# Kernel optimization log

Hardware: AMD Instinct MI355X
Metric: run time of the kernel (lower is better)

Reference implementation:

```python
import jax, jax.numpy as jnp
import numpy as np

NUM_HEADS = 4

def setup_inputs() -> dict:
    key = jax.random.key(0)
    ks = jax.random.split(key, 5)
    B, H, W, C = 4, 64, 64, 256
    x = jax.random.normal(ks[0], (B, H, W, C), dtype=jnp.float32)
    w_qkv = jax.random.normal(ks[1], (C, 3 * C), dtype=jnp.float32) * (C ** -0.5)
    b_qkv = jax.random.normal(ks[2], (3 * C,), dtype=jnp.float32) * 0.02
    w_out = jax.random.normal(ks[3], (C, C), dtype=jnp.float32) * (C ** -0.5)
    b_out = jax.random.normal(ks[4], (C,), dtype=jnp.float32) * 0.02
    return {"x": x, "w_qkv": w_qkv, "b_qkv": b_qkv, "w_out": w_out, "b_out": b_out}

def reference(x, w_qkv, b_qkv, w_out, b_out):
    B, H, W, C = x.shape
    nh = NUM_HEADS
    hd = C // nh
    scale = hd ** -0.5
    N = H * W
    # qkv projection: [B, N, 3, nh, hd]
    qkv = (x.reshape(B, N, C) @ w_qkv + b_qkv).reshape(B, N, 3, nh, hd)
    q, k, v = jnp.moveaxis(qkv, 2, 0)          # each [B, N, nh, hd]
    q = jnp.swapaxes(q, 1, 2)                  # [B, nh, N, hd]
    k = jnp.swapaxes(k, 1, 2)
    v = jnp.swapaxes(v, 1, 2)
    attn = jax.nn.softmax(jnp.einsum('bhnd,bhmd->bhnm', q * scale, k), axis=-1)
    o = jnp.einsum('bhnm,bhmd->bhnd', attn, v)  # [B, nh, N, hd]
    o = jnp.swapaxes(o, 1, 2).reshape(B, H, W, C)
    return o @ w_out + b_out
```

## Files before the change

### kernel.cpp

```cpp
#include <hip/hip_runtime.h>
#include <stdint.h>

typedef unsigned short u16;
typedef __attribute__((ext_vector_type(8))) short bf16x8;
typedef __attribute__((ext_vector_type(2))) float f32x2;
typedef __attribute__((ext_vector_type(4))) float f32x4;
typedef __attribute__((ext_vector_type(16))) float f32x16;

#define QSCL 0.1803368801111244f

#define GLD_LDS16(g, l) __builtin_amdgcn_global_load_lds( \
    (const __attribute__((address_space(1))) void*)(g),    \
    (__attribute__((address_space(3))) void*)(l), 16, 0, 0)

#if __has_builtin(__builtin_amdgcn_exp2f)
#define EXP2(x) __builtin_amdgcn_exp2f(x)
#else
#define EXP2(x) __builtin_exp2f(x)
#endif

__device__ __forceinline__ u16 f2bf(float f) {
    union { uint32_t i; float f; } v; v.f = f;
    uint32_t i = v.i;
    return (u16)((i + 0x7FFFu + ((i >> 16) & 1u)) >> 16);
}

__device__ __forceinline__ void p32swap(uint32_t& a, uint32_t& b) {
#if __has_builtin(__builtin_amdgcn_permlane32_swap)
    auto r = __builtin_amdgcn_permlane32_swap(a, b, false, false);
    a = (uint32_t)r[0]; b = (uint32_t)r[1];
#else
    const int hh = (int)((threadIdx.x & 63) >> 5);
    uint32_t ta = (uint32_t)__shfl_xor((int)a, 32);
    uint32_t tb = (uint32_t)__shfl_xor((int)b, 32);
    uint32_t na = hh ? tb : a;
    uint32_t nb = hh ? b : ta;
    a = na; b = nb;
#endif
}

__device__ __forceinline__ bf16x8 mk8(uint32_t a, uint32_t b, uint32_t c, uint32_t d) {
    union { uint32_t u[4]; bf16x8 v; } x;
    x.u[0] = a; x.u[1] = b; x.u[2] = c; x.u[3] = d;
    return x.v;
}

__device__ __forceinline__ void transpose_body(const float* __restrict__ src,
                                               u16* __restrict__ dst,
                                               int R, int Ctiles, int bid) {
    __shared__ u16 T[64][68];
    const int t = threadIdx.x;
    const int rt = bid / Ctiles;
    const int ct = bid % Ctiles;
    const int C = Ctiles << 6;

    for (int i = 0; i < 4; i++) {
        int idx = t + 256 * i;
        int row = idx >> 4;
        int col4 = (idx & 15) << 2;
        float4 d = *(const float4*)(src + (size_t)(rt * 64 + row) * C + ct * 64 + col4);
        T[col4 + 0][row] = f2bf(d.x);
        T[col4 + 1][row] = f2bf(d.y);
        T[col4 + 2][row] = f2bf(d.z);
        T[col4 + 3][row] = f2bf(d.w);
    }
    __syncthreads();
    for (int i = 0; i < 4; i++) {
        int idx = t + 256 * i;
        int row = idx >> 4;
        int col4 = (idx & 15) << 2;
        uint2 d = *(const uint2*)&T[row][col4];
        *(uint2*)(dst + (size_t)(ct * 64 + row) * R + rt * 64 + col4) = d;
    }
}

__global__ __launch_bounds__(256)
void transpose_kernel(const float* __restrict__ src, u16* __restrict__ dst,
                      int R, int Ctiles) {
    transpose_body(src, dst, R, Ctiles, blockIdx.x);
}

__global__ __launch_bounds__(256)
void prep_kernel(const float* __restrict__ w_qkv, u16* __restrict__ Wt,
                 const float* __restrict__ w_out, u16* __restrict__ Wt2,
                 const float* __restrict__ x, u16* __restrict__ xbf) {
    const int bid = blockIdx.x;
    if (bid < 48) {
        transpose_body(w_qkv, Wt, 256, 12, bid);
    } else if (bid < 64) {
        transpose_body(w_out, Wt2, 256, 4, bid - 48);
    } else {
        size_t i = ((size_t)(bid - 64) * 256 + threadIdx.x) * 4;
        float4 d = *(const float4*)(x + i);
        u16 e[4] = {f2bf(d.x), f2bf(d.y), f2bf(d.z), f2bf(d.w)};
        *(uint2*)(xbf + i) = *(uint2*)e;
    }
}

__global__ __launch_bounds__(256)
void gemm_qkv_old(const float* __restrict__ X, const u16* __restrict__ Wt,
                  const float* __restrict__ Bias, u16* __restrict__ QK,
                  u16* __restrict__ Vt) {
    __shared__ __align__(16) u16 As[64][40];
    __shared__ __align__(16) u16 Bts[64][40];

    const int t = threadIdx.x;
    const int lane = t & 63;
    const int wave = t >> 6;
    const int l15 = lane & 15;
    const int l4 = lane >> 4;

    const int ntile = blockIdx.x % 12;
    const int mbase = (blockIdx.x / 12) << 6;

    f32x4 acc[4];
    for (int c = 0; c < 4; c++) acc[c] = (f32x4){0.f, 0.f, 0.f, 0.f};

    for (int kc = 0; kc < 256; kc += 32) {
        __syncthreads();
        for (int i = 0; i < 2; i++) {
            int idx = t + 256 * i;
            int row = idx >> 3;
            int col4 = (idx & 7) << 2;
            float4 d = *(const float4*)(X + (size_t)(mbase + row) * 256 + kc + col4);
            u16 e[4] = {f2bf(d.x), f2bf(d.y), f2bf(d.z), f2bf(d.w)};
            *(uint2*)&As[row][col4] = *(uint2*)e;
        }
        for (int i = 0; i < 2; i++) {
            int idx = t + 256 * i;
            int row = idx >> 3;
            int col4 = (idx & 7) << 2;
            uint2 w = *(const uint2*)(Wt + (size_t)(ntile * 64 + row) * 256 + kc + col4);
            *(uint2*)&Bts[row][col4] = w;
        }
        __syncthreads();

        bf16x8 a = *(const bf16x8*)&As[wave * 16 + l15][l4 * 8];
        for (int c = 0; c < 4; c++) {
            bf16x8 b = *(const bf16x8*)&Bts[c * 16 + l15][l4 * 8];
            acc[c] = __builtin_amdgcn_mfma_f32_16x16x32_bf16(a, b, acc[c], 0, 0, 0);
        }
    }

    if (ntile < 8) {
        const float scl = (ntile < 4) ? QSCL : 1.0f;
        for (int c = 0; c < 4; c++) {
            int colc = c * 16 + l15;
            float bv = Bias[ntile * 64 + colc];
            for (int r = 0; r < 4; r++) {
                int row = mbase + wave * 16 + l4 * 4 + r;
                QK[(size_t)row * 512 + ntile * 64 + colc] = f2bf((acc[c][r] + bv) * scl);
            }
        }
    } else {
        const int h = ntile - 8;
        for (int c = 0; c < 4; c++) {
            int d = c * 16 + l15;
            float bv = Bias[512 + h * 64 + d];
            int n = mbase + wave * 16 + l4 * 4;
            int b = n >> 12;
            int nin = n & 4095;
            u16 e[4] = {f2bf(acc[c][0] + bv), f2bf(acc[c][1] + bv),
                        f2bf(acc[c][2] + bv), f2bf(acc[c][3] + bv)};
            *(uint2*)(Vt + ((size_t)(b * 4 + h) * 64 + d) * 4096 + nin) = *(uint2*)e;
        }
    }
}

__global__ __launch_bounds__(256)
void gemm_out_old(const u16* __restrict__ Wt2, const float* __restrict__ Bias,
                  float* __restrict__ IO) {
    __shared__ __align__(16) u16 As[64][264];
    __shared__ __align__(16) u16 Wts[256][40];

    const int t = threadIdx.x;
    const int lane = t & 63;
    const int wave = t >> 6;
    const int l15 = lane & 15;
    const int l4 = lane >> 4;
    const int mbase = blockIdx.x << 6;

    for (int i = 0; i < 16; i++) {
        int idx = t + 256 * i;
        int row = idx >> 6;
        int col4 = (idx & 63) << 2;
        float4 d = *(const float4*)(IO + (size_t)(mbase + row) * 256 + col4);
        u16 e[4] = {f2bf(d.x), f2bf(d.y), f2bf(d.z), f2bf(d.w)};
        *(uint2*)&As[row][col4] = *(uint2*)e;
    }

    f32x4 acc[4][4];
    for (int nt = 0; nt < 4; nt++)
        for (int c = 0; c < 4; c++) acc[nt][c] = (f32x4){0.f, 0.f, 0.f, 0.f};

    for (int kc = 0; kc < 256; kc += 32) {
        __syncthreads();
        for (int i = 0; i < 8; i++) {
            int idx = t + 256 * i;
            int row = idx >> 3;
            int col4 = (idx & 7) << 2;
            uint2 w = *(const uint2*)(Wt2 + (size_t)row * 256 + kc + col4);
            *(uint2*)&Wts[row][col4] = w;
        }
        __syncthreads();

        bf16x8 a = *(const bf16x8*)&As[wave * 16 + l15][kc + l4 * 8];
        for (int nt = 0; nt < 4; nt++)
            for (int c = 0; c < 4; c++) {
                bf16x8 b = *(const bf16x8*)&Wts[nt * 64 + c * 16 + l15][l4 * 8];
                acc[nt][c] = __builtin_amdgcn_mfma_f32_16x16x32_bf16(a, b, acc[nt][c], 0, 0, 0);
            }
    }

    for (int nt = 0; nt < 4; nt++)
        for (int c = 0; c < 4; c++) {
            int coln = nt * 64 + c * 16 + l15;
            float bv = Bias[coln];
            for (int r = 0; r < 4; r++) {
                int row = mbase + wave * 16 + l4 * 4 + r;
                IO[(size_t)row * 256 + coln] = acc[nt][c][r] + bv;
            }
        }
}

__global__ __launch_bounds__(256)
void gemm_qkv_new(const u16* __restrict__ Abf, const u16* __restrict__ Bt,
                  const float* __restrict__ Bias, u16* __restrict__ QK,
                  u16* __restrict__ Vt) {
    __shared__ __align__(16) u16 SM[24576];
    u16* Abuf = SM;
    u16* Bbuf = SM + 12288;

    const int t = threadIdx.x;
    const int lane = t & 63;
    const int wave = t >> 6;
    const int l15 = lane & 15;
    const int l4 = lane >> 4;
    const int wm = wave >> 1, wn = wave & 1;

    const int mb = blockIdx.x / 6;
    const int nb = blockIdx.x % 6;

    const u16* gA[2]; const u16* gB[2]; int ldsoff[2];
    #pragma unroll
    for (int i = 0; i < 2; i++) {
        int chunk = i * 256 + t;
        int row = chunk >> 2;
        int sch = (chunk & 3) ^ (row & 3);
        gA[i] = Abf + (size_t)(mb * 128 + row) * 256 + sch * 8;
        gB[i] = Bt + (size_t)(nb * 128 + row) * 256 + sch * 8;
        ldsoff[i] = (i * 256 + wave * 64) * 8;
    }
    int offA[4], offB[4];
    #pragma unroll
    for (int c = 0; c < 4; c++) {
        offA[c] = (wm * 64 + c * 16 + l15) * 32 + ((l4 ^ (l15 & 3)) * 8);
        offB[c] = (wn * 64 + c * 16 + l15) * 32 + ((l4 ^ (l15 & 3)) * 8);
    }

    f32x4 acc[4][4];
    #pragma unroll
    for (int cm = 0; cm < 4; cm++)
        for (int cn = 0; cn < 4; cn++) acc[cm][cn] = (f32x4){0.f, 0.f, 0.f, 0.f};

    auto stage = [&](int buf, int kc) {
        #pragma unroll
        for (int i = 0; i < 2; i++) {
            GLD_LDS16(gA[i] + kc, Abuf + buf * 4096 + ldsoff[i]);
            GLD_LDS16(gB[i] + kc, Bbuf + buf * 4096 + ldsoff[i]);
        }
    };

    stage(0, 0);
    stage(1, 32);
    #pragma unroll
    for (int s = 0; s < 8; ++s) {
        if (s == 7) asm volatile("s_waitcnt vmcnt(0)" ::: "memory");
        else        asm volatile("s_waitcnt vmcnt(4)" ::: "memory");
        __builtin_amdgcn_s_barrier();
        if (s < 6) stage((s + 2) % 3, (s + 2) * 32);

        const int rb = s % 3;
        bf16x8 a[4], b[4];
        #pragma unroll
        for (int c = 0; c < 4; c++) {
            a[c] = *(const bf16x8*)(Abuf + rb * 4096 + offA[c]);
            b[c] = *(const bf16x8*)(Bbuf + rb * 4096 + offB[c]);
        }
        #pragma unroll
        for (int cm = 0; cm < 4; cm++)
            #pragma unroll
            for (int cn = 0; cn < 4; cn++)
                acc[cm][cn] = __builtin_amdgcn_mfma_f32_16x16x32_bf16(
                    a[cm], b[cn], acc[cm][cn], 0, 0, 0);
    }

    __syncthreads();

    if (nb < 4) {
        #pragma unroll
        for (int cn = 0; cn < 4; cn++) {
            int lcol = wn * 64 + cn * 16 + l15;
            float bv = Bias[nb * 128 + lcol];
            float scl = ((nb * 2 + wn) < 4) ? QSCL : 1.0f;
            #pragma unroll
            for (int cm = 0; cm < 4; cm++) {
                int lr0 = wm * 64 + cm * 16 + l4 * 4;
                #pragma unroll
                for (int r = 0; r < 4; r++)
                    SM[(lr0 + r) * 136 + lcol] = f2bf((acc[cm][cn][r] + bv) * scl);
            }
        }
        __syncthreads();
        #pragma unroll
        for (int i = 0; i < 8; i++) {
            int c = t + 256 * i;
            int row = c >> 4;
            int off = (c & 15) * 8;
            uint4 v = *(const uint4*)&SM[row * 136 + off];
            *(uint4*)(QK + (size_t)(mb * 128 + row) * 512 + nb * 128 + off) = v;
        }
    } else {
        #pragma unroll
        for (int cn = 0; cn < 4; cn++) {
            int lcol = wn * 64 + cn * 16 + l15;
            float bv = Bias[nb * 128 + lcol];
            #pragma unroll
            for (int cm = 0; cm < 4; cm++) {
                int lr0 = wm * 64 + cm * 16 + l4 * 4;
                #pragma unroll
                for (int r = 0; r < 4; r++)
                    SM[lcol * 136 + lr0 + r] = f2bf(acc[cm][cn][r] + bv);
            }
        }
        __syncthreads();
        const int b_ = mb >> 5;
        const int nin0 = (mb * 128) & 4095;
        #pragma unroll
        for (int i = 0; i < 8; i++) {
            int c = t + 256 * i;
            int hd = c >> 4;
            int off = (c & 15) * 8;
            int h = (nb - 4) * 2 + (hd >> 6);
            int d = hd & 63;
            uint4 v = *(const uint4*)&SM[hd * 136 + off];
            *(uint4*)(Vt + ((size_t)(b_ * 4 + h) * 64 + d) * 4096 + nin0 + off) = v;
        }
    }
}

__global__ __launch_bounds__(256)
void gemm_out_new(const u16* __restrict__ Obf, const u16* __restrict__ Wt2,
                  const float* __restrict__ Bias, float* __restrict__ out) {
    __shared__ __align__(16) u16 SM[24576];
    u16* Abuf = SM;
    u16* Bbuf = SM + 12288;

    const int t = threadIdx.x;
    const int lane = t & 63;
    const int wave = t >> 6;
    const int l15 = lane & 15;
    const int l4 = lane >> 4;
    const int wm = wave >> 1, wn = wave & 1;

    const int mb = blockIdx.x >> 1;
    const int nb = blockIdx.x & 1;

    const u16* gA[2]; const u16* gB[2]; int ldsoff[2];
    #pragma unroll
    for (int i = 0; i < 2; i++) {
        int chunk = i * 256 + t;
        int row = chunk >> 2;
        int sch = (chunk & 3) ^ (row & 3);
        gA[i] = Obf + (size_t)(mb * 128 + row) * 256 + sch * 8;
        gB[i] = Wt2 + (size_t)(nb * 128 + row) * 256 + sch * 8;
        ldsoff[i] = (i * 256 + wave * 64) * 8;
    }
    int offA[4], offB[4];
    #pragma unroll
    for (int c = 0; c < 4; c++) {
        offA[c] = (wm * 64 + c * 16 + l15) * 32 + ((l4 ^ (l15 & 3)) * 8);
        offB[c] = (wn * 64 + c * 16 + l15) * 32 + ((l4 ^ (l15 & 3)) * 8);
    }

    f32x4 acc[4][4];
    #pragma unroll
    for (int cm = 0; cm < 4; cm++)
        for (int cn = 0; cn < 4; cn++) acc[cm][cn] = (f32x4){0.f, 0.f, 0.f, 0.f};

    auto stage = [&](int buf, int kc) {
        #pragma unroll
        for (int i = 0; i < 2; i++) {
            GLD_LDS16(gA[i] + kc, Abuf + buf * 4096 + ldsoff[i]);
            GLD_LDS16(gB[i] + kc, Bbuf + buf * 4096 + ldsoff[i]);
        }
    };

    stage(0, 0);
    stage(1, 32);
    #pragma unroll
    for (int s = 0; s < 8; ++s) {
        if (s == 7) asm volatile("s_waitcnt vmcnt(0)" ::: "memory");
        else        asm volatile("s_waitcnt vmcnt(4)" ::: "memory");
        __builtin_amdgcn_s_barrier();
        if (s < 6) stage((s + 2) % 3, (s + 2) * 32);

        const int rb = s % 3;
        bf16x8 a[4], b[4];
        #pragma unroll
        for (int c = 0; c < 4; c++) {
            a[c] = *(const bf16x8*)(Abuf + rb * 4096 + offA[c]);
            b[c] = *(const bf16x8*)(Bbuf + rb * 4096 + offB[c]);
        }
        #pragma unroll
        for (int cm = 0; cm < 4; cm++)
            #pragma unroll
            for (int cn = 0; cn < 4; cn++)
                acc[cm][cn] = __builtin_amdgcn_mfma_f32_16x16x32_bf16(
                    a[cm], b[cn], acc[cm][cn], 0, 0, 0);
    }

    float* F = (float*)SM;
    float bvv[4];
    #pragma unroll
    for (int cn = 0; cn < 4; cn++)
        bvv[cn] = Bias[nb * 128 + wn * 64 + cn * 16 + l15];

    #pragma unroll
    for (int p = 0; p < 2; p++) {
        __syncthreads();
        if (wm == p) {
            #pragma unroll
            for (int cn = 0; cn < 4; cn++) {
                int lcol = wn * 64 + cn * 16 + l15;
                #pragma unroll
                for (int cm = 0; cm < 4; cm++) {
                    int lr0 = cm * 16 + l4 * 4;
                    #pragma unroll
                    for (int r = 0; r < 4; r++)
                        F[(lr0 + r) * 136 + lcol] = acc[cm][cn][r] + bvv[cn];
                }
            }
        }
        __syncthreads();
        #pragma unroll
        for (int i = 0; i < 8; i++) {
            int c = t + 256 * i;
            int row = c >> 5;
            int off = (c & 31) * 4;
            float4 v = *(const float4*)&F[row * 136 + off];
            *(float4*)(out + (size_t)(mb * 128 + p * 64 + row) * 256 + nb * 128 + off) = v;
        }
    }
}

__global__ __launch_bounds__(256, 4)
void attn_kernel(const u16* __restrict__ QK, const u16* __restrict__ Vt,
                 float* __restrict__ Of, u16* __restrict__ Obf, int writebf,
                 int bhmask, int bhbits) {
    __shared__ __align__(16) u16 Kt[2][64][64];
    __shared__ __align__(16) u16 Vts[2][64][64];

    const int t = threadIdx.x;
    const int lane = t & 63;
    const int wave = t >> 6;
    const int l31 = lane & 31;
    const int h = lane >> 5;
    const int jw = wave & 1;
    const int qw = wave >> 1;

    const int bh = blockIdx.x & bhmask;
    const int qb = blockIdx.x >> bhbits;
    const int b = bh >> 2;
    const int hd = bh & 3;

    const size_t qkbase = (size_t)b * 4096 * 512;
    const size_t vtbase = (size_t)bh * 64 * 4096;
    const int q = qb * 64 + qw * 32 + l31;

    const u16* gk[2]; const u16* gv[2]; u16* lk[2]; u16* lv[2];
    #pragma unroll
    for (int i = 0; i < 2; i++) {
        int ck = i * 256 + t;
        int row = ck >> 3;
        int sch = (ck & 7) ^ (row & 7);
        gk[i] = QK + qkbase + (size_t)row * 512 + 256 + hd * 64 + sch * 8;
        gv[i] = Vt + vtbase + (size_t)row * 4096 + sch * 8;
        lk[i] = &Kt[0][0][0] + (i * 256 + wave * 64) * 8;
        lv[i] = &Vts[0][0][0] + (i * 256 + wave * 64) * 8;
    }

    int kfo[4];
    {
        int row = jw * 32 + l31;
        int sw = row & 7;
        #pragma unroll
        for (int dc = 0; dc < 4; dc++)
            kfo[dc] = row * 64 + ((dc * 2 + h) ^ sw) * 8;
    }
    int vfo[2][2];
    #pragma unroll
    for (int dh = 0; dh < 2; dh++) {
        int row = dh * 32 + l31;
        int sw = row & 7;
        #pragma unroll
        for (int J = 0; J < 2; J++)
            vfo[dh][J] = row * 64 + ((jw * 4 + J * 2 + h) ^ sw) * 8;
    }

    bf16x8 qf[4];
    #pragma unroll
    for (int dc = 0; dc < 4; dc++)
        qf[dc] = *(const bf16x8*)(QK + qkbase + (size_t)q * 512
                                  + hd * 64 + dc * 16 + h * 8);

    const f32x16 z16 = {0.f, 0.f, 0.f, 0.f, 0.f, 0.f, 0.f, 0.f,
                        0.f, 0.f, 0.f, 0.f, 0.f, 0.f, 0.f, 0.f};
    f32x16 Oacc[2];
    Oacc[0] = z16; Oacc[1] = z16;
    f32x2 lsum2 = {0.f, 0.f};

    auto stageKV = [&](int buf, int jn) {
        #pragma unroll
        for (int i = 0; i < 2; i++) {
            GLD_LDS16(gk[i] + (size_t)jn * 32768, lk[i] + buf * 4096);
            GLD_LDS16(gv[i] + jn * 64,            lv[i] + buf * 4096);
        }
    };

    auto body = [&](int par, int jn) {
        __syncthreads();
        stageKV(par ^ 1, jn);

        const u16* kb = &Kt[0][0][0] + par * 4096;
        const u16* vb = &Vts[0][0][0] + par * 4096;

        bf16x8 kf0 = *(const bf16x8*)(kb + kfo[0]);
        bf16x8 kf1 = *(const bf16x8*)(kb + kfo[1]);
        bf16x8 kf2 = *(const bf16x8*)(kb + kfo[2]);
        bf16x8 kf3 = *(const bf16x8*)(kb + kfo[3]);

        f32x16 s;
        s = __builtin_amdgcn_mfma_f32_32x32x16_bf16(kf0, qf[0], z16, 0, 0, 0);
        s = __builtin_amdgcn_mfma_f32_32x32x16_bf16(kf1, qf[1], s, 0, 0, 0);
        s = __builtin_amdgcn_mfma_f32_32x32x16_bf16(kf2, qf[2], s, 0, 0, 0);
        s = __builtin_amdgcn_mfma_f32_32x32x16_bf16(kf3, qf[3], s, 0, 0, 0);

        bf16x8 vf00 = *(const bf16x8*)(vb + vfo[0][0]);
        bf16x8 vf01 = *(const bf16x8*)(vb + vfo[0][1]);
        bf16x8 vf10 = *(const bf16x8*)(vb + vfo[1][0]);
        bf16x8 vf11 = *(const bf16x8*)(vb + vfo[1][1]);

        uint32_t w[8];
        f32x2 ls2 = {0.f, 0.f};
        #pragma unroll
        for (int k = 0; k < 8; k++) {
            float p0 = EXP2(s[2 * k]);
            float p1 = EXP2(s[2 * k + 1]);
            ls2 += (f32x2){p0, p1};
            asm("v_cvt_pk_bf16_f32 %0, %1, %2" : "=v"(w[k]) : "v"(p0), "v"(p1));
        }
        lsum2 += ls2;

        p32swap(w[0], w[2]); p32swap(w[1], w[3]);
        p32swap(w[4], w[6]); p32swap(w[5], w[7]);

        bf16x8 bp0 = mk8(w[0], w[1], w[2], w[3]);
        bf16x8 bp1 = mk8(w[4], w[5], w[6], w[7]);

        Oacc[0] = __builtin_amdgcn_mfma_f32_32x32x16_bf16(vf00, bp0, Oacc[0], 0, 0, 0);
        Oacc[0] = __builtin_amdgcn_mfma_f32_32x32x16_bf16(vf01, bp1, Oacc[0], 0, 0, 0);
        Oacc[1] = __builtin_amdgcn_mfma_f32_32x32x16_bf16(vf10, bp0, Oacc[1], 0, 0, 0);
        Oacc[1] = __builtin_amdgcn_mfma_f32_32x32x16_bf16(vf11, bp1, Oacc[1], 0, 0, 0);
    };

    stageKV(0, 0);
    for (int jt = 0; jt < 64; jt += 2) {
        body(0, jt + 1);
        body(1, (jt + 2) & 63);
    }

    float lsum = lsum2[0] + lsum2[1];
    lsum += __shfl_xor(lsum, 32);

    __syncthreads();
    float* sc  = (float*)&Kt[0][0][0];
    float* scl = (float*)&Vts[0][0][0];
    const int swl = lane & 7;

    if (jw) {
        float* ob = sc + qw * 2048 + lane * 32;
        #pragma unroll
        for (int dh = 0; dh < 2; dh++)
            #pragma unroll
            for (int i = 0; i < 4; i++) {
                int k8 = dh * 4 + i;
                f32x4 c = {Oacc[dh][4 * i + 0], Oacc[dh][4 * i + 1],
                           Oacc[dh][4 * i + 2], Oacc[dh][4 * i + 3]};
                *(f32x4*)(ob + ((k8 ^ swl) * 4)) = c;
            }
        scl[qw * 64 + lane] = lsum;
    }
    __syncthreads();
    if (!jw) {
        float* ob = sc + qw * 2048 + lane * 32;
        float lt = lsum + scl[qw * 64 + lane];
        float inv = 1.f / lt;
        size_t row = (size_t)b * 4096 + q;
        #pragma unroll
        for (int dh = 0; dh < 2; dh++)
            #pragma unroll
            for (int i = 0; i < 4; i++) {
                int k8 = dh * 4 + i;
                f32x4 pR = *(f32x4*)(ob + ((k8 ^ swl) * 4));
                f32x4 o;
                #pragma unroll
                for (int r = 0; r < 4; r++)
                    o[r] = (Oacc[dh][4 * i + r] + pR[r]) * inv;
                int col = hd * 64 + dh * 32 + i * 8 + h * 4;
                if (writebf) {
                    u16 e[4] = {f2bf(o[0]), f2bf(o[1]), f2bf(o[2]), f2bf(o[3])};
                    *(uint2*)(Obf + row * 256 + col) = *(uint2*)e;
                } else {
                    *(f32x4*)(Of + row * 256 + col) = o;
                }
            }
    }
}

extern "C" void kernel_launch(void* const* d_in, const int* in_sizes, int n_in,
                              void* d_out, int out_size, void* d_ws, size_t ws_size,
                              hipStream_t stream) {
    const float* x     = (const float*)d_in[0];
    const float* w_qkv = (const float*)d_in[1];
    const float* b_qkv = (const float*)d_in[2];
    const float* w_out = (const float*)d_in[3];
    const float* b_out = (const float*)d_in[4];
    float* out = (float*)d_out;

    char* ws = (char*)d_ws;
    u16* Wt  = (u16*)ws;
    u16* Wt2 = (u16*)(ws + 393216);
    u16* QK  = (u16*)(ws + 524288);
    u16* Vt  = (u16*)(ws + 524288 + 16777216);
    u16* XO  = (u16*)(ws + 524288 + 16777216 + 8388608);
    const size_t NEED_NEW = 524288 + 16777216 + 8388608 + 8388608;

    if (ws_size >= NEED_NEW) {
        prep_kernel<<<dim3(4160), dim3(256), 0, stream>>>(w_qkv, Wt, w_out, Wt2, x, XO);
        gemm_qkv_new<<<dim3(768), dim3(256), 0, stream>>>(XO, Wt, b_qkv, QK, Vt);
        attn_kernel<<<dim3(1024), dim3(256), 0, stream>>>(
            QK, Vt, out, XO, 1, 15, 4);
        gemm_out_new<<<dim3(256), dim3(256), 0, stream>>>(XO, Wt2, b_out, out);
    } else {
        transpose_kernel<<<dim3(48), dim3(256), 0, stream>>>(w_qkv, Wt, 256, 12);
        transpose_kernel<<<dim3(16), dim3(256), 0, stream>>>(w_out, Wt2, 256, 4);
        gemm_qkv_old<<<dim3(3072), dim3(256), 0, stream>>>(x, Wt, b_qkv, QK, Vt);
        attn_kernel<<<dim3(1024), dim3(256), 0, stream>>>(
            QK, Vt, out, (u16*)nullptr, 0, 15, 4);
        gemm_out_old<<<dim3(256), dim3(256), 0, stream>>>(Wt2, b_out, out);
    }
}
```

Before: 183.4 us.

## Load K/V fragments directly from global into registers, dropping LDS staging

Replaces the double-buffered LDS staging of K and V tiles (global_load_lds plus a __syncthreads per tile) with direct per-lane global vector loads into MFMA fragment registers. K for the next tile is prefetched into registers while the current tile computes. V is loaded inside each iteration. This removes the per-iteration barriers and most LDS use, which may raise occupancy. In exchange, waves with the same jw now load the same K/V data separately, loads become less coalesced (strided rows), and more registers are needed.

```diff
diff --git a/kernel.cpp b/kernel.cpp
--- a/kernel.cpp
+++ b/kernel.cpp
@@ -458,8 +458,7 @@
 void attn_kernel(const u16* __restrict__ QK, const u16* __restrict__ Vt,
                  float* __restrict__ Of, u16* __restrict__ Obf, int writebf,
                  int bhmask, int bhbits) {
-    __shared__ __align__(16) u16 Kt[2][64][64];
-    __shared__ __align__(16) u16 Vts[2][64][64];
+    __shared__ __align__(16) float SC[4224];
 
     const int t = threadIdx.x;
     const int lane = t & 63;
@@ -478,35 +477,8 @@
     const size_t vtbase = (size_t)bh * 64 * 4096;
     const int q = qb * 64 + qw * 32 + l31;
 
-    const u16* gk[2]; const u16* gv[2]; u16* lk[2]; u16* lv[2];
-    #pragma unroll
-    for (int i = 0; i < 2; i++) {
-        int ck = i * 256 + t;
-        int row = ck >> 3;
-        int sch = (ck & 7) ^ (row & 7);
-        gk[i] = QK + qkbase + (size_t)row * 512 + 256 + hd * 64 + sch * 8;
-        gv[i] = Vt + vtbase + (size_t)row * 4096 + sch * 8;
-        lk[i] = &Kt[0][0][0] + (i * 256 + wave * 64) * 8;
-        lv[i] = &Vts[0][0][0] + (i * 256 + wave * 64) * 8;
-    }
-
-    int kfo[4];
-    {
-        int row = jw * 32 + l31;
-        int sw = row & 7;
-        #pragma unroll
-        for (int dc = 0; dc < 4; dc++)
-            kfo[dc] = row * 64 + ((dc * 2 + h) ^ sw) * 8;
-    }
-    int vfo[2][2];
-    #pragma unroll
-    for (int dh = 0; dh < 2; dh++) {
-        int row = dh * 32 + l31;
-        int sw = row & 7;
-        #pragma unroll
-        for (int J = 0; J < 2; J++)
-            vfo[dh][J] = row * 64 + ((jw * 4 + J * 2 + h) ^ sw) * 8;
-    }
+    const u16* kp0 = QK + qkbase + (size_t)(jw * 32 + l31) * 512 + 256 + hd * 64 + h * 8;
+    const u16* vp0 = Vt + vtbase + (size_t)l31 * 4096 + jw * 32 + h * 8;
 
     bf16x8 qf[4];
     #pragma unroll
@@ -520,36 +492,30 @@
     Oacc[0] = z16; Oacc[1] = z16;
     f32x2 lsum2 = {0.f, 0.f};
 
-    auto stageKV = [&](int buf, int jn) {
-        #pragma unroll
-        for (int i = 0; i < 2; i++) {
-            GLD_LDS16(gk[i] + (size_t)jn * 32768, lk[i] + buf * 4096);
-            GLD_LDS16(gv[i] + jn * 64,            lv[i] + buf * 4096);
-        }
+    auto loadK = [&](bf16x8* k, int jt) {
+        const u16* p = kp0 + ((size_t)jt << 15);
+        #pragma unroll
+        for (int dc = 0; dc < 4; dc++)
+            k[dc] = *(const bf16x8*)(p + dc * 16);
     };
-
-    auto body = [&](int par, int jn) {
-        __syncthreads();
-        stageKV(par ^ 1, jn);
-
-        const u16* kb = &Kt[0][0][0] + par * 4096;
-        const u16* vb = &Vts[0][0][0] + par * 4096;
-
-        bf16x8 kf0 = *(const bf16x8*)(kb + kfo[0]);
-        bf16x8 kf1 = *(const bf16x8*)(kb + kfo[1]);
-        bf16x8 kf2 = *(const bf16x8*)(kb + kfo[2]);
-        bf16x8 kf3 = *(const bf16x8*)(kb + kfo[3]);
+    auto loadV = [&](bf16x8* v, int jt) {
+        const u16* p = vp0 + jt * 64;
+        v[0] = *(const bf16x8*)(p);
+        v[1] = *(const bf16x8*)(p + 16);
+        v[2] = *(const bf16x8*)(p + 32 * 4096);
+        v[3] = *(const bf16x8*)(p + 32 * 4096 + 16);
+    };
+
+    auto body = [&](bf16x8* kc, bf16x8* kn, int jtv, int jtn) {
+        bf16x8 vf[4];
+        loadV(vf, jtv);
+        loadK(kn, jtn);
 
         f32x16 s;
-        s = __builtin_amdgcn_mfma_f32_32x32x16_bf16(kf0, qf[0], z16, 0, 0, 0);
-        s = __builtin_amdgcn_mfma_f32_32x32x16_bf16(kf1, qf[1], s, 0, 0, 0);
-        s = __builtin_amdgcn_mfma_f32_32x32x16_bf16(kf2, qf[2], s, 0, 0, 0);
-        s = __builtin_amdgcn_mfma_f32_32x32x16_bf16(kf3, qf[3], s, 0, 0, 0);
-
-        bf16x8 vf00 = *(const bf16x8*)(vb + vfo[0][0]);
-        bf16x8 vf01 = *(const bf16x8*)(vb + vfo[0][1]);
-        bf16x8 vf10 = *(const bf16x8*)(vb + vfo[1][0]);
-        bf16x8 vf11 = *(const bf16x8*)(vb + vfo[1][1]);
+        s = __builtin_amdgcn_mfma_f32_32x32x16_bf16(kc[0], qf[0], z16, 0, 0, 0);
+        s = __builtin_amdgcn_mfma_f32_32x32x16_bf16(kc[1], qf[1], s, 0, 0, 0);
+        s = __builtin_amdgcn_mfma_f32_32x32x16_bf16(kc[2], qf[2], s, 0, 0, 0);
+        s = __builtin_amdgcn_mfma_f32_32x32x16_bf16(kc[3], qf[3], s, 0, 0, 0);
 
         uint32_t w[8];
         f32x2 ls2 = {0.f, 0.f};
@@ -568,26 +534,27 @@
         bf16x8 bp0 = mk8(w[0], w[1], w[2], w[3]);
         bf16x8 bp1 = mk8(w[4], w[5], w[6], w[7]);
 
-        Oacc[0] = __builtin_amdgcn_mfma_f32_32x32x16_bf16(vf00, bp0, Oacc[0], 0, 0, 0);
-        Oacc[0] = __builtin_amdgcn_mfma_f32_32x32x16_bf16(vf01, bp1, Oacc[0], 0, 0, 0);
-        Oacc[1] = __builtin_amdgcn_mfma_f32_32x32x16_bf16(vf10, bp0, Oacc[1], 0, 0, 0);
-        Oacc[1] = __builtin_amdgcn_mfma_f32_32x32x16_bf16(vf11, bp1, Oacc[1], 0, 0, 0);
+        Oacc[0] = __builtin_amdgcn_mfma_f32_32x32x16_bf16(vf[0], bp0, Oacc[0], 0, 0, 0);
+        Oacc[0] = __builtin_amdgcn_mfma_f32_32x32x16_bf16(vf[1], bp1, Oacc[0], 0, 0, 0);
+        Oacc[1] = __builtin_amdgcn_mfma_f32_32x32x16_bf16(vf[2], bp0, Oacc[1], 0, 0, 0);
+        Oacc[1] = __builtin_amdgcn_mfma_f32_32x32x16_bf16(vf[3], bp1, Oacc[1], 0, 0, 0);
     };
 
-    stageKV(0, 0);
+    bf16x8 k0[4], k1[4];
+    loadK(k0, 0);
     for (int jt = 0; jt < 64; jt += 2) {
-        body(0, jt + 1);
-        body(1, (jt + 2) & 63);
+        body(k0, k1, jt, jt + 1);
+        body(k1, k0, jt + 1, (jt + 2) & 63);
     }
 
     float lsum = lsum2[0] + lsum2[1];
     lsum += __shfl_xor(lsum, 32);
 
+    float* sc  = SC;
+    float* scl = SC + 4096;
+    const int swl = lane & 7;
+
     __syncthreads();
-    float* sc  = (float*)&Kt[0][0][0];
-    float* scl = (float*)&Vts[0][0][0];
-    const int swl = lane & 7;
-
     if (jw) {
         float* ob = sc + qw * 2048 + lane * 32;
         #pragma unroll
```

Result: slower. 330.2 us (+80.0%).
